# Kernel tuning notes

Measured on AMD Instinct MI355X. Metric: run time of the kernel, lower is better.

The kernel has to match this reference:

```python
import jax, jax.numpy as jnp
import numpy as np
from jax import lax


def _gauss1d(size, sigma):
    k = np.arange(size, dtype=np.float32) - (size - 1) / 2.0
    k = np.exp(-0.5 * (k / sigma) ** 2)
    return k / k.sum()


def _make_kernel(scale, sigma):
    # make_odd
    kx, ky, kz = [s + 1 if s % 2 == 0 else s for s in scale]
    kH = _gauss1d(kx, sigma)
    kW = _gauss1d(ky, sigma)
    kD = _gauss1d(kz, sigma)
    kern = kH[:, None, None] * kW[None, :, None] * kD[None, None, :]  # (kx, ky, kz)
    kern = np.transpose(kern, (2, 0, 1))  # permute(2,0,1) -> (kz, kx, ky)
    return jnp.asarray(kern, dtype=jnp.float32)


def setup_inputs() -> dict:
    key = jax.random.key(0)
    x = jax.random.normal(key, (2, 1, 256, 256, 256), dtype=jnp.float32)
    kernel0 = _make_kernel((2, 2, 2), 1.0)  # (3,3,3)
    kernel1 = _make_kernel((4, 4, 4), 1.0)  # (5,5,5)
    return {"x": x, "kernel0": kernel0, "kernel1": kernel1}


def _blur_down(x, kernel, stride):
    # replicate pad by k//2 per spatial dim, then depthwise (C=1) conv3d.
    pad = [(0, 0), (0, 0)] + [(k // 2, k // 2) for k in kernel.shape]
    xp = jnp.pad(x, pad, mode='edge')
    # strided VALID conv == full blur followed by [::s] slicing (output ceil(H/s))
    return lax.conv_general_dilated(
        xp, kernel[None, None].astype(x.dtype),
        window_strides=stride, padding='VALID',
        dimension_numbers=('NCDHW', 'OIDHW', 'NCDHW'))


def reference(x, kernel0, kernel1):
    d1 = _blur_down(x, kernel0, (2, 2, 2))  # (2,1,128,128,128)
    d2 = _blur_down(x, kernel1, (4, 4, 4))  # (2,1,64,64,64)
    return (x, d1, d2)
```

## Files before the change

### kernel.cpp

```cpp
#include <hip/hip_runtime.h>

#define S_IN 256
#define S_D1 128
#define S_D2 64
#define IN_PER_BATCH (S_IN * S_IN * S_IN)
#define D1_PER_BATCH (S_D1 * S_D1 * S_D1)
#define D2_PER_BATCH (S_D2 * S_D2 * S_D2)
#define X_ELEMS (2 * IN_PER_BATCH)
#define D1_ELEMS (2 * D1_PER_BATCH)
#define D2_ELEMS (2 * D2_PER_BATCH)

#define TD 8
#define TH 8
#define TW 64
#define LZ (TD + 4)
#define LY (TH + 4)
#define LX (TW + 8)
#define LDS_ELEMS (LZ * LY * LX)

__global__ __launch_bounds__(256) void fused_pyramid(
    const float* __restrict__ x, const float* __restrict__ k0,
    const float* __restrict__ k1, float* __restrict__ out0,
    float* __restrict__ out1, float* __restrict__ out2)
{
    __shared__ float ls[LDS_ELEMS];
    __shared__ float kw0[27];
    __shared__ float kw1[125];

    const int tid = threadIdx.x;
    if (tid < 27) kw0[tid] = k0[tid];
    else if (tid >= 32 && tid < 32 + 125) kw1[tid - 32] = k1[tid - 32];

    const int bx = blockIdx.x;
    const int wt = bx & 3;
    const int hy = (bx >> 2) & 31;
    const int dz = (bx >> 7) & 31;
    const int n  = bx >> 12;

    const int x0 = wt * TW;
    const int y0 = hy * TH;
    const int z0 = dz * TD;

    const float* xb = x + (size_t)n * IN_PER_BATCH;

    for (int v = tid; v < 144 * 18; v += 256) {
        int row = v / 18;
        int j   = v - row * 18;
        int lz  = row / LY;
        int ly  = row - lz * LY;
        int gz = z0 + lz - 2; gz = gz < 0 ? 0 : (gz > S_IN - 1 ? S_IN - 1 : gz);
        int gy = y0 + ly - 2; gy = gy < 0 ? 0 : (gy > S_IN - 1 ? S_IN - 1 : gy);
        const float* rp = xb + ((size_t)gz * S_IN + gy) * S_IN;
        int gx = x0 - 4 + 4 * j;
        float4 val;
        if (gx >= 0 && gx <= S_IN - 4) {
            val = *reinterpret_cast<const float4*>(rp + gx);
        } else {
            float s = rp[gx < 0 ? 0 : (S_IN - 1)];
            val = make_float4(s, s, s, s);
        }
        *reinterpret_cast<float4*>(&ls[(lz * LY + ly) * LX + 4 * j]) = val;
    }
    __syncthreads();

    {
        float* ob0 = out0 + (size_t)n * IN_PER_BATCH;
#pragma unroll
        for (int i = 0; i < 4; ++i) {
            int v   = tid + 256 * i;
            int row = v >> 4;
            int j   = v & 15;
            int lz  = row >> 3;
            int ly  = row & 7;
            float4 val = *reinterpret_cast<const float4*>(
                &ls[((lz + 2) * LY + (ly + 2)) * LX + 4 + 4 * j]);
            int gz = z0 + lz, gy = y0 + ly, gxo = x0 + 4 * j;
            *reinterpret_cast<float4*>(
                &ob0[((size_t)gz * S_IN + gy) * S_IN + gxo]) = val;
        }
    }

    {
        float* ob1 = out1 + (size_t)n * D1_PER_BATCH;
        const int ox  = tid & 31;
        const int oy  = (tid >> 5) & 3;
        const int ozb = tid >> 7;
#pragma unroll
        for (int it = 0; it < 2; ++it) {
            int oz = ozb + 2 * it;
            float acc = 0.0f;
#pragma unroll
            for (int a = 0; a < 3; ++a) {
                int lz = 2 * oz + a + 1;
#pragma unroll
                for (int b = 0; b < 3; ++b) {
                    int ly = 2 * oy + b + 1;
                    const float* lr = &ls[(lz * LY + ly) * LX + 2 * ox + 3];
                    const float* kr = &kw0[(a * 3 + b) * 3];
                    acc = fmaf(kr[0], lr[0], acc);
                    acc = fmaf(kr[1], lr[1], acc);
                    acc = fmaf(kr[2], lr[2], acc);
                }
            }
            int d = dz * 4 + oz, h = hy * 4 + oy, w = wt * 32 + ox;
            ob1[((size_t)d * S_D1 + h) * S_D1 + w] = acc;
        }
    }

    {
        float* ob2 = out2 + (size_t)n * D2_PER_BATCH;
        const int q  = tid & 3;
        const int o  = tid >> 2;
        const int ox = o & 15;
        const int oy = (o >> 4) & 1;
        const int oz = o >> 5;
        float acc = 0.0f;
        for (int a = q; a < 5; a += 4) {
            int lz = 4 * oz + a;
#pragma unroll
            for (int b = 0; b < 5; ++b) {
                int ly = 4 * oy + b;
                const float* lr = &ls[(lz * LY + ly) * LX + 4 * ox + 2];
                const float* kr = &kw1[(a * 5 + b) * 5];
#pragma unroll
                for (int c = 0; c < 5; ++c)
                    acc = fmaf(kr[c], lr[c], acc);
            }
        }
        acc += __shfl_xor(acc, 1);
        acc += __shfl_xor(acc, 2);
        if (q == 0) {
            int d = dz * 2 + oz, h = hy * 2 + oy, w = wt * 16 + ox;
            ob2[((size_t)d * S_D2 + h) * S_D2 + w] = acc;
        }
    }
}

extern "C" void kernel_launch(void* const* d_in, const int* in_sizes, int n_in,
                              void* d_out, int out_size, void* d_ws, size_t ws_size,
                              hipStream_t stream) {
    const float* x  = (const float*)d_in[0];
    const float* k0 = (const float*)d_in[1];
    const float* k1 = (const float*)d_in[2];

    float* out0 = (float*)d_out;
    float* out1 = out0 + X_ELEMS;
    float* out2 = out1 + D1_ELEMS;

    const int blocks = 4 * 32 * 32 * 2;
    fused_pyramid<<<blocks, 256, 0, stream>>>(x, k0, k1, out0, out1, out2);
}
```

Baseline: 338.6 us.

## Halve tile width, stage loads in registers, remap blocks, vectorize LDS reads

The x-tile width drops from 64 to 32, doubling the number of blocks, and block IDs are remapped with a stride-8 swizzle (intended to spread work across XCDs). Global loads are first collected into registers, then written both to LDS and directly to the x-copy output, so the copy no longer reads back from LDS. The d1 and d2 convolutions use float2/float4 LDS reads, and the d2 reduction is split over 8 lanes. The narrower tile raises the halo-to-interior ratio, which adds redundant global reads.

```diff
diff --git a/kernel.cpp b/kernel.cpp
--- a/kernel.cpp
+++ b/kernel.cpp
@@ -12,10 +12,11 @@
 
 #define TD 8
 #define TH 8
-#define TW 64
-#define LZ (TD + 4)
-#define LY (TH + 4)
-#define LX (TW + 8)
+#define TW 32
+#define LZ 12
+#define LY 12
+#define LX 40
+#define NV (LZ * LY * (LX / 4))
 #define LDS_ELEMS (LZ * LY * LX)
 
 __global__ __launch_bounds__(256) void fused_pyramid(
@@ -29,108 +30,117 @@
 
     const int tid = threadIdx.x;
     if (tid < 27) kw0[tid] = k0[tid];
-    else if (tid >= 32 && tid < 32 + 125) kw1[tid - 32] = k1[tid - 32];
+    else if (tid >= 32 && tid < 157) kw1[tid - 32] = k1[tid - 32];
 
     const int bx = blockIdx.x;
-    const int wt = bx & 3;
-    const int hy = (bx >> 2) & 31;
-    const int dz = (bx >> 7) & 31;
-    const int n  = bx >> 12;
+    const int lin = (bx & 7) * 2048 + (bx >> 3);
+    const int wt = lin & 7;
+    const int hy = (lin >> 3) & 31;
+    const int dz = (lin >> 8) & 31;
+    const int n  = lin >> 13;
 
     const int x0 = wt * TW;
     const int y0 = hy * TH;
     const int z0 = dz * TD;
 
     const float* xb = x + (size_t)n * IN_PER_BATCH;
+    float* ob0 = out0 + (size_t)n * IN_PER_BATCH;
+    float* ob1 = out1 + (size_t)n * D1_PER_BATCH;
+    float* ob2 = out2 + (size_t)n * D2_PER_BATCH;
 
-    for (int v = tid; v < 144 * 18; v += 256) {
-        int row = v / 18;
-        int j   = v - row * 18;
-        int lz  = row / LY;
-        int ly  = row - lz * LY;
-        int gz = z0 + lz - 2; gz = gz < 0 ? 0 : (gz > S_IN - 1 ? S_IN - 1 : gz);
-        int gy = y0 + ly - 2; gy = gy < 0 ? 0 : (gy > S_IN - 1 ? S_IN - 1 : gy);
-        const float* rp = xb + ((size_t)gz * S_IN + gy) * S_IN;
-        int gx = x0 - 4 + 4 * j;
-        float4 val;
-        if (gx >= 0 && gx <= S_IN - 4) {
-            val = *reinterpret_cast<const float4*>(rp + gx);
-        } else {
-            float s = rp[gx < 0 ? 0 : (S_IN - 1)];
-            val = make_float4(s, s, s, s);
+    float4 vals[6];
+#pragma unroll
+    for (int i = 0; i < 6; ++i) {
+        int v = tid + (i << 8);
+        if (v < NV) {
+            int row = v / 10;
+            int j   = v - row * 10;
+            int lz  = row / LY;
+            int ly  = row - lz * LY;
+            int gz = z0 + lz - 2; gz = gz < 0 ? 0 : (gz > 255 ? 255 : gz);
+            int gy = y0 + ly - 2; gy = gy < 0 ? 0 : (gy > 255 ? 255 : gy);
+            const float* rp = xb + ((size_t)gz * S_IN + gy) * S_IN;
+            int gx = x0 - 4 + (j << 2);
+            if (gx >= 0 && gx <= S_IN - 4) {
+                vals[i] = *reinterpret_cast<const float4*>(rp + gx);
+            } else {
+                float s = rp[gx < 0 ? 0 : (S_IN - 1)];
+                vals[i] = make_float4(s, s, s, s);
+            }
         }
-        *reinterpret_cast<float4*>(&ls[(lz * LY + ly) * LX + 4 * j]) = val;
+    }
+#pragma unroll
+    for (int i = 0; i < 6; ++i) {
+        int v = tid + (i << 8);
+        if (v < NV) {
+            int row = v / 10;
+            int j   = v - row * 10;
+            int lz  = row / LY;
+            int ly  = row - lz * LY;
+            *reinterpret_cast<float4*>(&ls[(lz * LY + ly) * LX + (j << 2)]) = vals[i];
+            if ((unsigned)(lz - 2) < 8u && (unsigned)(ly - 2) < 8u &&
+                (unsigned)(j - 1) < 8u) {
+                int gz = z0 + lz - 2, gy = y0 + ly - 2, gx = x0 - 4 + (j << 2);
+                *reinterpret_cast<float4*>(
+                    &ob0[((size_t)gz * S_IN + gy) * S_IN + gx]) = vals[i];
+            }
+        }
     }
     __syncthreads();
 
     {
-        float* ob0 = out0 + (size_t)n * IN_PER_BATCH;
+        const int ox = tid & 15;
+        const int oy = (tid >> 4) & 3;
+        const int oz = tid >> 6;
+        float acc = 0.0f;
 #pragma unroll
-        for (int i = 0; i < 4; ++i) {
-            int v   = tid + 256 * i;
-            int row = v >> 4;
-            int j   = v & 15;
-            int lz  = row >> 3;
-            int ly  = row & 7;
-            float4 val = *reinterpret_cast<const float4*>(
-                &ls[((lz + 2) * LY + (ly + 2)) * LX + 4 + 4 * j]);
-            int gz = z0 + lz, gy = y0 + ly, gxo = x0 + 4 * j;
-            *reinterpret_cast<float4*>(
-                &ob0[((size_t)gz * S_IN + gy) * S_IN + gxo]) = val;
+        for (int a = 0; a < 3; ++a) {
+            int lz = 2 * oz + 1 + a;
+#pragma unroll
+            for (int b = 0; b < 3; ++b) {
+                int ly = 2 * oy + 1 + b;
+                const float* base = &ls[(lz * LY + ly) * LX + 2 * ox + 2];
+                float2 v0 = *reinterpret_cast<const float2*>(base);
+                float2 v1 = *reinterpret_cast<const float2*>(base + 2);
+                const float* kr = &kw0[(a * 3 + b) * 3];
+                acc = fmaf(kr[0], v0.y, acc);
+                acc = fmaf(kr[1], v1.x, acc);
+                acc = fmaf(kr[2], v1.y, acc);
+            }
         }
+        int d = 4 * dz + oz, h = 4 * hy + oy, w = 16 * wt + ox;
+        ob1[((size_t)d * S_D1 + h) * S_D1 + w] = acc;
     }
 
     {
-        float* ob1 = out1 + (size_t)n * D1_PER_BATCH;
-        const int ox  = tid & 31;
-        const int oy  = (tid >> 5) & 3;
-        const int ozb = tid >> 7;
+        const int q = tid & 7;
+        const int o = tid >> 3;
+        const int ox = o & 7;
+        const int oy = (o >> 3) & 1;
+        const int oz = o >> 4;
+        float acc = 0.0f;
 #pragma unroll
-        for (int it = 0; it < 2; ++it) {
-            int oz = ozb + 2 * it;
-            float acc = 0.0f;
-#pragma unroll
-            for (int a = 0; a < 3; ++a) {
-                int lz = 2 * oz + a + 1;
-#pragma unroll
-                for (int b = 0; b < 3; ++b) {
-                    int ly = 2 * oy + b + 1;
-                    const float* lr = &ls[(lz * LY + ly) * LX + 2 * ox + 3];
-                    const float* kr = &kw0[(a * 3 + b) * 3];
-                    acc = fmaf(kr[0], lr[0], acc);
-                    acc = fmaf(kr[1], lr[1], acc);
-                    acc = fmaf(kr[2], lr[2], acc);
-                }
-            }
-            int d = dz * 4 + oz, h = hy * 4 + oy, w = wt * 32 + ox;
-            ob1[((size_t)d * S_D1 + h) * S_D1 + w] = acc;
-        }
-    }
-
-    {
-        float* ob2 = out2 + (size_t)n * D2_PER_BATCH;
-        const int q  = tid & 3;
-        const int o  = tid >> 2;
-        const int ox = o & 15;
-        const int oy = (o >> 4) & 1;
-        const int oz = o >> 5;
-        float acc = 0.0f;
-        for (int a = q; a < 5; a += 4) {
-            int lz = 4 * oz + a;
-#pragma unroll
-            for (int b = 0; b < 5; ++b) {
-                int ly = 4 * oy + b;
-                const float* lr = &ls[(lz * LY + ly) * LX + 4 * ox + 2];
-                const float* kr = &kw1[(a * 5 + b) * 5];
-#pragma unroll
-                for (int c = 0; c < 5; ++c)
-                    acc = fmaf(kr[c], lr[c], acc);
+        for (int m = 0; m < 4; ++m) {
+            int r = q + (m << 3);
+            if (r < 25) {
+                int a = r / 5, b = r - 5 * a;
+                int lz = 4 * oz + a, ly = 4 * oy + b;
+                const float* base = &ls[(lz * LY + ly) * LX + 4 * ox];
+                float4 A = *reinterpret_cast<const float4*>(base);
+                float4 B = *reinterpret_cast<const float4*>(base + 4);
+                const float* kr = &kw1[r * 5];
+                acc = fmaf(kr[0], A.z, acc);
+                acc = fmaf(kr[1], A.w, acc);
+                acc = fmaf(kr[2], B.x, acc);
+                acc = fmaf(kr[3], B.y, acc);
+                acc = fmaf(kr[4], B.z, acc);
             }
         }
         acc += __shfl_xor(acc, 1);
         acc += __shfl_xor(acc, 2);
+        acc += __shfl_xor(acc, 4);
         if (q == 0) {
-            int d = dz * 2 + oz, h = hy * 2 + oy, w = wt * 16 + ox;
+            int d = 2 * dz + oz, h = 2 * hy + oy, w = 8 * wt + ox;
             ob2[((size_t)d * S_D2 + h) * S_D2 + w] = acc;
         }
     }
@@ -147,6 +157,6 @@
     float* out1 = out0 + X_ELEMS;
     float* out2 = out1 + D1_ELEMS;
 
-    const int blocks = 4 * 32 * 32 * 2;
+    const int blocks = 8 * 32 * 32 * 2;
     fused_pyramid<<<blocks, 256, 0, stream>>>(x, k0, k1, out0, out1, out2);
 }
```

Measured after the change: 303.7 us. 10.3% less time.
